# Kernel optimization log

Hardware: AMD Instinct MI355X
Metric: run time of the kernel (lower is better)

## Reference

```python
import jax, jax.numpy as jnp
import numpy as np

B_SZ, SEQ, IN_F, OUT_F, ST_F = 16, 4096, 256, 256, 256
RMIN, RMAX, MAX_PHASE = 0.9, 1.0, 6.283


def setup_inputs() -> dict:
    key = jax.random.key(0)
    ks = jax.random.split(key, 8)
    u1 = jax.random.uniform(ks[0], (ST_F,))
    u2 = jax.random.uniform(ks[1], (ST_F,))
    # same init math as the torch module
    nu_log = jnp.log(-0.5 * jnp.log(u1 * (RMAX + RMIN) * (RMAX - RMIN) + RMIN ** 2))
    theta_log = jnp.log(MAX_PHASE * u2)
    lam_abs = jnp.exp(-jnp.exp(nu_log))
    gamma_log = jnp.log(jnp.sqrt(1.0 - lam_abs ** 2))
    s2in = np.sqrt(2.0 * IN_F)
    B_re = jax.random.normal(ks[2], (ST_F, IN_F)) / s2in
    B_im = jax.random.normal(ks[3], (ST_F, IN_F)) / s2in
    sst = np.sqrt(ST_F)
    C_re = jax.random.normal(ks[4], (OUT_F, ST_F)) / sst
    C_im = jax.random.normal(ks[5], (OUT_F, ST_F)) / sst
    D = jax.random.normal(ks[6], (OUT_F, IN_F)) / np.sqrt(IN_F)
    inp = jax.random.normal(ks[7], (B_SZ, SEQ, IN_F), dtype=jnp.float32)
    return {"input": inp, "nu_log": nu_log, "theta_log": theta_log,
            "gamma_log": gamma_log, "B_re": B_re, "B_im": B_im,
            "C_re": C_re, "C_im": C_im, "D": D}


def _binop(a, b):
    # diagonal linear recurrence combine: (A, Bu)
    return (a[0] * b[0], b[0] * a[1] + b[1])


def reference(input, nu_log, theta_log, gamma_log, B_re, B_im, C_re, C_im, D):
    lam_abs = jnp.exp(-jnp.exp(nu_log))
    lam = (lam_abs * jnp.exp(1j * jnp.exp(theta_log))).astype(jnp.complex64)  # [N]
    gam = jnp.exp(gamma_log)[:, None]                                        # [N,1]
    Bm = (gam * (B_re + 1j * B_im)).astype(jnp.complex64)                    # [N,Hin]
    Cm = (C_re + 1j * C_im).astype(jnp.complex64)                            # [Hout,N]
    # Bu_t = B @ u_t  -> [B,L,N]
    Bu = jnp.einsum('blh,nh->bln', input.astype(jnp.complex64), Bm)
    lam_el = jnp.broadcast_to(lam, Bu.shape)
    # parallel associative scan over time: s_t = lam*s_{t-1} + Bu_t, s_{-1}=0
    _, s = jax.lax.associative_scan(_binop, (lam_el, Bu), axis=1)
    # module records the state BEFORE each update (initial state is zero)
    zero0 = jnp.zeros((input.shape[0], 1, lam.shape[0]), dtype=jnp.complex64)
    inner_states = jnp.concatenate([zero0, s[:, :-1, :]], axis=1)            # [B,L,N]
    output = jnp.einsum('bln,on->blo', inner_states, Cm).real \
             + jnp.einsum('blh,oh->blo', input, D)
    return output, inner_states
```

## Files before the change

kernel.cpp:

```cpp
#include <hip/hip_runtime.h>


typedef float  f32x4 __attribute__((ext_vector_type(4)));
typedef short  s16x8 __attribute__((ext_vector_type(8)));

__device__ __forceinline__ unsigned short f2bf(float x) {
  unsigned int u = __builtin_bit_cast(unsigned int, x);
  u += 0x7FFFu + ((u >> 16) & 1u);
  return (unsigned short)(u >> 16);
}
__device__ __forceinline__ float bf2f(unsigned int s) {
  unsigned int u = s << 16;
  return __builtin_bit_cast(float, u);
}
__device__ __forceinline__ f32x4 mfma16(s16x8 a, s16x8 b, f32x4 c) {
  return __builtin_amdgcn_mfma_f32_16x16x32_bf16(a, b, c, 0, 0, 0);
}

__global__ void k0_mix(const float* __restrict__ nu_log, const float* __restrict__ theta_log,
                       const float* __restrict__ gamma_log,
                       const float* __restrict__ B_re, const float* __restrict__ B_im,
                       const float* __restrict__ C_re, const float* __restrict__ C_im,
                       const float* __restrict__ Dm,
                       unsigned short* __restrict__ W1, float* __restrict__ W2f,
                       float* __restrict__ lamre, float* __restrict__ lamim,
                       float* __restrict__ lamLre, float* __restrict__ lamLim) {
  int idx = blockIdx.x * 256 + threadIdx.x;
  if (idx < 131072) {
    int ki = idx & 31; int np_ = (idx >> 5) & 511; int kk = idx >> 14;
    int k = kk * 32 + ki; int n = np_ & 255;
    float g = expf(gamma_log[n]);
    float v = (np_ < 256) ? B_re[n * 256 + k] : B_im[n * 256 + k];
    W1[idx] = f2bf(g * v);
  } else if (idx < 327680) {
    int j = idx - 131072;
    int k = j >> 8, o = j & 255;
    float v;
    if (k < 512) { int n = k >> 1; v = (k & 1) ? -C_im[o * 256 + n] : C_re[o * 256 + n]; }
    else         { v = Dm[o * 256 + (k - 512)]; }
    W2f[j] = v;
  } else if (idx < 327936) {
    int n = idx - 327680;
    float la = expf(-expf(nu_log[n]));
    float th = expf(theta_log[n]);
    float lr = la * cosf(th), li = la * sinf(th);
    lamre[n] = lr; lamim[n] = li;
    float r = lr, i = li;
    #pragma unroll
    for (int t = 0; t < 5; ++t) { float nr = r * r - i * i; float ni = 2.f * r * i; r = nr; i = ni; }
    lamLre[n] = r; lamLim[n] = i;
  }
}

__global__ void k0b_tile(const float* __restrict__ W2f, unsigned short* __restrict__ W2t) {
  int j = blockIdx.x * 256 + threadIdx.x;
  int ki = j & 31, o = (j >> 5) & 255, kk = j >> 13;
  W2t[j] = f2bf(W2f[(kk * 32 + ki) * 256 + o]);
}

__global__ __launch_bounds__(1024, 4) void k1_bstat(const float* __restrict__ in,
                                                    const unsigned short* __restrict__ W1,
                                                    unsigned int* __restrict__ BuP,
                                                    const float* __restrict__ lamre,
                                                    const float* __restrict__ lamim,
                                                    float2* __restrict__ cl) {
  __shared__ unsigned short lA[64 * 264];
  int tid = threadIdx.x, lane = tid & 63, w = tid >> 6;
  int l15 = lane & 15, q = lane >> 4;
  int n = w * 16 + l15;
  size_t row0 = (size_t)blockIdx.x * 64;

  s16x8 breg[2][2][2];
  auto loadB = [&](int buf, int ph) {
    #pragma unroll
    for (int p = 0; p < 2; ++p)
      #pragma unroll
      for (int t = 0; t < 2; ++t) {
        int kk = ph * 2 + t;
        breg[buf][p][t] = *reinterpret_cast<const s16x8*>(
            W1 + (size_t)(kk * 512 + p * 256 + n) * 32 + q * 8);
      }
  };

  loadB(0, 0);

  #pragma unroll
  for (int i = 0; i < 4; ++i) {
    int chunk = i * 1024 + tid;
    int m = chunk >> 6, h0 = (chunk & 63) * 4;
    float4 v = *reinterpret_cast<const float4*>(in + (row0 + m) * 256 + h0);
    ushort4 s; s.x = f2bf(v.x); s.y = f2bf(v.y); s.z = f2bf(v.z); s.w = f2bf(v.w);
    *reinterpret_cast<ushort4*>(&lA[m * 264 + h0]) = s;
  }
  __syncthreads();

  f32x4 acc[4][2];
  #pragma unroll
  for (int mt = 0; mt < 4; ++mt)
    #pragma unroll
    for (int p = 0; p < 2; ++p) acc[mt][p] = f32x4{0.f, 0.f, 0.f, 0.f};

  #pragma unroll
  for (int ph = 0; ph < 4; ++ph) {
    const int cur = ph & 1;
    if (ph < 3) loadB(cur ^ 1, ph + 1);
    #pragma unroll
    for (int t = 0; t < 2; ++t) {
      int kk = ph * 2 + t;
      #pragma unroll
      for (int mt = 0; mt < 4; ++mt) {
        s16x8 af = *reinterpret_cast<const s16x8*>(
            &lA[(mt * 16 + l15) * 264 + kk * 32 + q * 8]);
        acc[mt][0] = mfma16(af, breg[cur][0][t], acc[mt][0]);
        acc[mt][1] = mfma16(af, breg[cur][1][t], acc[mt][1]);
      }
    }
  }

  #pragma unroll
  for (int mt = 0; mt < 4; ++mt)
    #pragma unroll
    for (int r = 0; r < 4; ++r) {
      size_t row = row0 + mt * 16 + q * 4 + r;
      unsigned int pk = (unsigned int)f2bf(acc[mt][0][r]) |
                        ((unsigned int)f2bf(acc[mt][1][r]) << 16);
      BuP[row * 256 + n] = pk;
    }

  {
    float lr = lamre[n], li = lamim[n];
    float l2r = lr * lr - li * li, l2i = 2.f * lr * li;
    float l4r = l2r * l2r - l2i * l2i, l4i = 2.f * l2r * l2i;
    float p8r = l4r * l4r - l4i * l4i, p8i = 2.f * l4r * l4i;
    float p12r = p8r * l4r - p8i * l4i, p12i = p8r * l4i + p8i * l4r;
    float p16r = p8r * p8r - p8i * p8i, p16i = 2.f * p8r * p8i;
    float e1r, e1i;
    if (q == 0)      { e1r = p12r; e1i = p12i; }
    else if (q == 1) { e1r = p8r;  e1i = p8i;  }
    else if (q == 2) { e1r = l4r;  e1i = l4i;  }
    else             { e1r = 1.f;  e1i = 0.f;  }
    float e0r = e1r * p16r - e1i * p16i;
    float e0i = e1r * p16i + e1i * p16r;
    #pragma unroll
    for (int ch = 0; ch < 2; ++ch) {
      float hr[2], hi[2];
      #pragma unroll
      for (int h = 0; h < 2; ++h) {
        int mt = ch * 2 + h;
        float xr = 0.f, xi = 0.f;
        #pragma unroll
        for (int r = 0; r < 4; ++r) {
          float br = acc[mt][0][r], bi2 = acc[mt][1][r];
          float nr2 = lr * xr - li * xi + br;
          float ni2 = lr * xi + li * xr + bi2;
          xr = nr2; xi = ni2;
        }
        hr[h] = xr; hi[h] = xi;
      }
      float Tr = e0r * hr[0] - e0i * hi[0] + e1r * hr[1] - e1i * hi[1];
      float Ti = e0r * hi[0] + e0i * hr[0] + e1r * hi[1] + e1i * hr[1];
      Tr += __shfl_xor(Tr, 16); Ti += __shfl_xor(Ti, 16);
      Tr += __shfl_xor(Tr, 32); Ti += __shfl_xor(Ti, 32);
      if (q == 0) {
        size_t C = (size_t)blockIdx.x * 2 + ch;
        cl[C * 256 + n] = make_float2(Tr, Ti);
      }
    }
  }
}

__global__ void k2b_scan(const float2* __restrict__ cl, float2* __restrict__ cin,
                         const float* __restrict__ lamLre, const float* __restrict__ lamLim) {
  int b = blockIdx.x, n = threadIdx.x;
  float lr = lamLre[n], li = lamLim[n];
  float sr = 0.f, si = 0.f;
  #pragma unroll 4
  for (int c = 0; c < 128; ++c) {
    size_t idx = ((size_t)b * 128 + c) * 256 + n;
    float2 L = cl[idx];
    cin[idx] = make_float2(sr, si);
    float nr = lr * sr - li * si + L.x;
    float ni = lr * si + li * sr + L.y;
    sr = nr; si = ni;
  }
}

__global__ __launch_bounds__(256) void k3a_scan(unsigned int* BuP, float* __restrict__ innerRe,
                                                const float2* __restrict__ cin,
                                                const float* __restrict__ lamre,
                                                const float* __restrict__ lamim) {
  int b = blockIdx.x >> 7, c = blockIdx.x & 127, n = threadIdx.x;
  size_t row0 = (size_t)b * 4096 + c * 32;
  float2 s0 = cin[((size_t)b * 128 + c) * 256 + n];
  float sr = s0.x, si = s0.y;
  float lr = lamre[n], li = lamim[n];
  #pragma unroll 4
  for (int j = 0; j < 32; ++j) {
    size_t idx = (row0 + j) * 256 + n;
    unsigned int v = BuP[idx];
    BuP[idx] = (unsigned int)f2bf(sr) | ((unsigned int)f2bf(si) << 16);
    innerRe[idx] = sr;
    float br = bf2f(v & 0xffffu), bi = bf2f(v >> 16);
    float nr = lr * sr - li * si + br;
    float ni = lr * si + li * sr + bi;
    sr = nr; si = ni;
  }
}

__global__ __launch_bounds__(1024, 4) void k3b_breg(const float* __restrict__ in,
                                                    const unsigned short* SPack,
                                                    const unsigned short* __restrict__ W2t,
                                                    float* outp) {
  __shared__ unsigned short lA[64 * 776];
  int tid = threadIdx.x, lane = tid & 63, w = tid >> 6;
  int l15 = lane & 15, q = lane >> 4;
  size_t row0 = (size_t)blockIdx.x * 64;

  s16x8 breg[2][4];
  auto loadB = [&](int buf, int p) {
    #pragma unroll
    for (int t = 0; t < 4; ++t) {
      int kk = p * 4 + t;
      int c = w * 16 + l15;
      breg[buf][t] = *reinterpret_cast<const s16x8*>(
          W2t + ((size_t)kk * 256 + c) * 32 + q * 8);
    }
  };

  loadB(0, 0);

  #pragma unroll
  for (int i = 0; i < 4; ++i) {
    int chunk = i * 1024 + tid;
    int r = chunk >> 6, c8 = (chunk & 63) * 8;
    *reinterpret_cast<uint4*>(&lA[r * 776 + c8]) =
        *reinterpret_cast<const uint4*>(SPack + (row0 + r) * 512 + c8);
  }
  #pragma unroll
  for (int i = 0; i < 4; ++i) {
    int chunk = i * 1024 + tid;
    int m = chunk >> 6, h0 = (chunk & 63) * 4;
    float4 v = *reinterpret_cast<const float4*>(in + (row0 + m) * 256 + h0);
    ushort4 s; s.x = f2bf(v.x); s.y = f2bf(v.y); s.z = f2bf(v.z); s.w = f2bf(v.w);
    *reinterpret_cast<ushort4*>(&lA[m * 776 + 512 + h0]) = s;
  }
  __syncthreads();

  f32x4 acc[4];
  #pragma unroll
  for (int mt = 0; mt < 4; ++mt) acc[mt] = f32x4{0.f, 0.f, 0.f, 0.f};

  #pragma unroll
  for (int p = 0; p < 6; ++p) {
    const int cur = p & 1;
    if (p < 5) loadB(cur ^ 1, p + 1);
    #pragma unroll
    for (int t = 0; t < 4; ++t) {
      int kk = p * 4 + t;
      #pragma unroll
      for (int mt = 0; mt < 4; ++mt) {
        s16x8 af = *reinterpret_cast<const s16x8*>(
            &lA[(mt * 16 + l15) * 776 + kk * 32 + q * 8]);
        acc[mt] = mfma16(af, breg[cur][t], acc[mt]);
      }
    }
  }

  #pragma unroll
  for (int mt = 0; mt < 4; ++mt)
    #pragma unroll
    for (int r = 0; r < 4; ++r) {
      size_t row = row0 + mt * 16 + q * 4 + r;
      int col = w * 16 + l15;
      outp[row * 256 + col] = acc[mt][r];
    }
}

extern "C" void kernel_launch(void* const* d_in, const int* in_sizes, int n_in,
                              void* d_out, int out_size, void* d_ws, size_t ws_size,
                              hipStream_t stream) {
  (void)in_sizes; (void)n_in; (void)out_size;
  const float* in       = (const float*)d_in[0];
  const float* nu_log   = (const float*)d_in[1];
  const float* theta_log= (const float*)d_in[2];
  const float* gamma_log= (const float*)d_in[3];
  const float* B_re     = (const float*)d_in[4];
  const float* B_im     = (const float*)d_in[5];
  const float* C_re     = (const float*)d_in[6];
  const float* C_im     = (const float*)d_in[7];
  const float* Dm       = (const float*)d_in[8];

  if (ws_size < (size_t)10 * 1024 * 1024) return;
  char* ws = (char*)d_ws;
  unsigned short* W1 = (unsigned short*)(ws + 0);
  float* W2f   = (float*)(ws + 262144);
  float* lamre  = (float*)(ws + 1048576);
  float* lamim  = lamre + 256;
  float* lamLre = lamre + 512;
  float* lamLim = lamre + 768;
  unsigned short* W2t = (unsigned short*)(ws + 1310720);
  float2* cl  = (float2*)(ws + (size_t)2 * 1024 * 1024);
  float2* cin = (float2*)(ws + (size_t)6 * 1024 * 1024);

  unsigned int* BuP = (unsigned int*)d_out;
  float* innerRe = (float*)d_out + (size_t)16777216;

  k0_mix<<<1281, 256, 0, stream>>>(nu_log, theta_log, gamma_log, B_re, B_im, C_re, C_im, Dm,
                                   W1, W2f, lamre, lamim, lamLre, lamLim);
  k0b_tile<<<768, 256, 0, stream>>>(W2f, W2t);
  k1_bstat<<<1024, 1024, 0, stream>>>(in, W1, BuP, lamre, lamim, cl);
  k2b_scan<<<16, 256, 0, stream>>>(cl, cin, lamLre, lamLim);
  k3a_scan<<<2048, 256, 0, stream>>>(BuP, innerRe, cin, lamre, lamim);
  k3b_breg<<<1024, 1024, 0, stream>>>(in, (const unsigned short*)BuP, W2t, (float*)BuP);
}
```

Before: 146.1 us.

## Retile output GEMM to 32-row blocks with 4 waves covering 64 columns each

Rewrites the final output GEMM kernel to use 256-thread blocks over 32 rows instead of 1024-thread blocks over 64 rows. Each wave now computes a 32x64 tile (2x4 MFMA tiles), so every A fragment read from LDS is reused across four column tiles, which cuts LDS traffic per MFMA. The trade-off is more B-register traffic per block, since each wave loads 64 columns of W2t, and more registers per thread. Smaller blocks and less shared memory per block may also help occupancy and scheduling.

```diff
diff --git a/kernel.cpp b/kernel.cpp
--- a/kernel.cpp
+++ b/kernel.cpp
@@ -207,38 +207,40 @@
   }
 }
 
-__global__ __launch_bounds__(1024, 4) void k3b_breg(const float* __restrict__ in,
-                                                    const unsigned short* SPack,
-                                                    const unsigned short* __restrict__ W2t,
-                                                    float* outp) {
-  __shared__ unsigned short lA[64 * 776];
+__global__ __launch_bounds__(256, 4) void k3b_breg(const float* __restrict__ in,
+                                                   const unsigned short* SPack,
+                                                   const unsigned short* __restrict__ W2t,
+                                                   float* outp) {
+  __shared__ unsigned short lA[32 * 776];
   int tid = threadIdx.x, lane = tid & 63, w = tid >> 6;
   int l15 = lane & 15, q = lane >> 4;
-  size_t row0 = (size_t)blockIdx.x * 64;
-
-  s16x8 breg[2][4];
-  auto loadB = [&](int buf, int p) {
-    #pragma unroll
-    for (int t = 0; t < 4; ++t) {
-      int kk = p * 4 + t;
-      int c = w * 16 + l15;
-      breg[buf][t] = *reinterpret_cast<const s16x8*>(
-          W2t + ((size_t)kk * 256 + c) * 32 + q * 8);
-    }
+  size_t row0 = (size_t)blockIdx.x * 32;
+
+  s16x8 breg[2][4][2];
+  auto loadB = [&](int buf, int ph) {
+    #pragma unroll
+    for (int ct = 0; ct < 4; ++ct)
+      #pragma unroll
+      for (int t = 0; t < 2; ++t) {
+        int kk = ph * 2 + t;
+        int c = w * 64 + ct * 16 + l15;
+        breg[buf][ct][t] = *reinterpret_cast<const s16x8*>(
+            W2t + ((size_t)kk * 256 + c) * 32 + q * 8);
+      }
   };
 
   loadB(0, 0);
 
   #pragma unroll
-  for (int i = 0; i < 4; ++i) {
-    int chunk = i * 1024 + tid;
+  for (int i = 0; i < 8; ++i) {
+    int chunk = i * 256 + tid;
     int r = chunk >> 6, c8 = (chunk & 63) * 8;
     *reinterpret_cast<uint4*>(&lA[r * 776 + c8]) =
         *reinterpret_cast<const uint4*>(SPack + (row0 + r) * 512 + c8);
   }
   #pragma unroll
-  for (int i = 0; i < 4; ++i) {
-    int chunk = i * 1024 + tid;
+  for (int i = 0; i < 8; ++i) {
+    int chunk = i * 256 + tid;
     int m = chunk >> 6, h0 = (chunk & 63) * 4;
     float4 v = *reinterpret_cast<const float4*>(in + (row0 + m) * 256 + h0);
     ushort4 s; s.x = f2bf(v.x); s.y = f2bf(v.y); s.z = f2bf(v.z); s.w = f2bf(v.w);
@@ -246,34 +248,40 @@
   }
   __syncthreads();
 
-  f32x4 acc[4];
-  #pragma unroll
-  for (int mt = 0; mt < 4; ++mt) acc[mt] = f32x4{0.f, 0.f, 0.f, 0.f};
-
-  #pragma unroll
-  for (int p = 0; p < 6; ++p) {
-    const int cur = p & 1;
-    if (p < 5) loadB(cur ^ 1, p + 1);
-    #pragma unroll
-    for (int t = 0; t < 4; ++t) {
-      int kk = p * 4 + t;
-      #pragma unroll
-      for (int mt = 0; mt < 4; ++mt) {
+  f32x4 acc[2][4];
+  #pragma unroll
+  for (int mt = 0; mt < 2; ++mt)
+    #pragma unroll
+    for (int ct = 0; ct < 4; ++ct) acc[mt][ct] = f32x4{0.f, 0.f, 0.f, 0.f};
+
+  #pragma unroll
+  for (int ph = 0; ph < 12; ++ph) {
+    const int cur = ph & 1;
+    if (ph < 11) loadB(cur ^ 1, ph + 1);
+    #pragma unroll
+    for (int t = 0; t < 2; ++t) {
+      int kk = ph * 2 + t;
+      #pragma unroll
+      for (int mt = 0; mt < 2; ++mt) {
         s16x8 af = *reinterpret_cast<const s16x8*>(
             &lA[(mt * 16 + l15) * 776 + kk * 32 + q * 8]);
-        acc[mt] = mfma16(af, breg[cur][t], acc[mt]);
+        #pragma unroll
+        for (int ct = 0; ct < 4; ++ct)
+          acc[mt][ct] = mfma16(af, breg[cur][ct][t], acc[mt][ct]);
       }
     }
   }
 
   #pragma unroll
-  for (int mt = 0; mt < 4; ++mt)
-    #pragma unroll
-    for (int r = 0; r < 4; ++r) {
-      size_t row = row0 + mt * 16 + q * 4 + r;
-      int col = w * 16 + l15;
-      outp[row * 256 + col] = acc[mt][r];
-    }
+  for (int mt = 0; mt < 2; ++mt)
+    #pragma unroll
+    for (int ct = 0; ct < 4; ++ct)
+      #pragma unroll
+      for (int r = 0; r < 4; ++r) {
+        size_t row = row0 + mt * 16 + q * 4 + r;
+        int col = w * 64 + ct * 16 + l15;
+        outp[row * 256 + col] = acc[mt][ct][r];
+      }
 }
 
 extern "C" void kernel_launch(void* const* d_in, const int* in_sizes, int n_in,
@@ -311,5 +319,5 @@
   k1_bstat<<<1024, 1024, 0, stream>>>(in, W1, BuP, lamre, lamim, cl);
   k2b_scan<<<16, 256, 0, stream>>>(cl, cin, lamLre, lamLim);
   k3a_scan<<<2048, 256, 0, stream>>>(BuP, innerRe, cin, lamre, lamim);
-  k3b_breg<<<1024, 1024, 0, stream>>>(in, (const unsigned short*)BuP, W2t, (float*)BuP);
-}
+  k3b_breg<<<2048, 256, 0, stream>>>(in, (const unsigned short*)BuP, W2t, (float*)BuP);
+}
```

Result: slower. 151.8 us (+3.9%).
